# Performance work log

Hardware: AMD Instinct MI355X
Metric: run time of the kernel (lower is better)

## Reference

```python
import jax, jax.numpy as jnp
import numpy as np

EPS = 1e-5
T = 5          # Newton-Schulz iterations
G = 64         # num_groups
FACTOR = 1.0   # reparameterization scale


def setup_inputs() -> dict:
    key = jax.random.key(0)
    k1, k2, k3, k4 = jax.random.split(key, 4)
    B, C, H, W = 32, 256, 64, 64
    x = jax.random.normal(k1, (B, C, H, W), dtype=jnp.float32)
    idx = jax.random.permutation(k2, C)                      # random channel shuffle
    eps1 = jax.random.normal(k3, (B, G, G), dtype=jnp.float32)  # randn_like(wm_inv)
    eps2 = jax.random.normal(k4, (B, G, 1), dtype=jnp.float32)  # randn_like(mean)
    return {"x": x, "idx": idx, "eps1": eps1, "eps2": eps2}


def _sqrtvar(t):
    # torch .var(dim=0) is unbiased (ddof=1); repeat over batch == broadcast
    return jnp.sqrt(jnp.var(t, axis=0, keepdims=True, ddof=1) + EPS)


def reference(x, idx, eps1, eps2):
    B, C, H, W = x.shape
    # reverse permutation: reverse_idx[idx[i]] = i
    reverse_idx = jnp.zeros_like(idx).at[idx].set(jnp.arange(C, dtype=idx.dtype))

    xs = x[:, idx].reshape(B, G, -1)          # [B, G, m], m = (C//G)*H*W
    m = xs.shape[-1]
    mean = xs.mean(-1, keepdims=True)         # [B, G, 1]
    xm = xs - mean

    sigma = jnp.einsum('bgm,bhm->bgh', xm, xm) / m   # [B, G, G]
    I = jnp.eye(G, dtype=x.dtype)
    trace_inv = 1.0 / jnp.trace(sigma, axis1=1, axis2=2)[:, None, None]
    sigma_N = sigma * trace_inv

    # Newton-Schulz inverse square root: P <- 1.5 P - 0.5 P^3 sigma_N
    P = jnp.broadcast_to(I, sigma.shape)
    for _ in range(T):
        P = 1.5 * P - 0.5 * ((P @ P @ P) @ sigma_N)
    wm = P * jnp.sqrt(trace_inv)

    # faithful to original b_inv: solve(I, wm) == wm (original code quirk)
    wm_inv = jnp.linalg.solve(jnp.broadcast_to(I, wm.shape), wm)

    # stochastic reparameterization of gamma (symmetrized via triu) and beta
    wir = wm_inv + (eps1 * FACTOR) * _sqrtvar(wm_inv)
    gamma = jnp.triu(wir) + jnp.swapaxes(jnp.triu(wir, k=1), 1, 2)
    beta = mean + (eps2 * FACTOR) * _sqrtvar(mean)

    y = gamma @ (wm @ xm) + beta              # [B, G, m]
    out = y.reshape(B, C, H, W)[:, reverse_idx]
    return out
```

## Files before the change

### kernel.cpp

```cpp
#include <hip/hip_runtime.h>

typedef __attribute__((ext_vector_type(8))) short short8;
typedef __attribute__((ext_vector_type(4))) short short4v;
typedef __attribute__((ext_vector_type(4))) float f32x4;

#define MFMA16 __builtin_amdgcn_mfma_f32_16x16x32_bf16

__device__ __forceinline__ short bf16t(float f) {
  return (short)(__float_as_uint(f) >> 16);
}
__device__ __forceinline__ float bf16f(short h) {
  return __uint_as_float(((unsigned)(unsigned short)h) << 16);
}

__device__ __forceinline__ void mm64(const float* X, const float* Y, float* D,
                                     int tid) {
  const int R = (tid >> 4) << 2;
  const int Cc = (tid & 15) << 2;
  float acc[4][4];
#pragma unroll
  for (int i = 0; i < 4; i++)
#pragma unroll
    for (int j = 0; j < 4; j++) acc[i][j] = 0.f;
#pragma unroll 4
  for (int kk = 0; kk < 64; kk++) {
    f32x4 a = *(const f32x4*)&X[(kk << 6) + R];
    f32x4 bb = *(const f32x4*)&Y[(kk << 6) + Cc];
#pragma unroll
    for (int i = 0; i < 4; i++)
#pragma unroll
      for (int j = 0; j < 4; j++) acc[i][j] = fmaf(a[i], bb[j], acc[i][j]);
  }
#pragma unroll
  for (int i = 0; i < 4; i++) {
    f32x4 r = {acc[i][0], acc[i][1], acc[i][2], acc[i][3]};
    *(f32x4*)&D[((R + i) << 6) + Cc] = r;
  }
  __syncthreads();
}

__global__ __launch_bounds__(256, 4) void k_stats(const float* __restrict__ x,
                                                  const int* __restrict__ idx,
                                                  float* __restrict__ sigw,
                                                  float* __restrict__ rsum) {
  __shared__ __align__(16) short XT[2][2 * 64 * 72];
  __shared__ int chan[64];
  const int tid = threadIdx.x;
  const int w = tid >> 6, lane = tid & 63;
  const int q = lane >> 4, n15 = lane & 15;
  const int u = tid >> 4;
  const int quad = tid & 15;
  const int blk = blockIdx.x;
  const int b = blk >> 5, k = (blk >> 3) & 3, pc = blk & 7;

  if (tid < 64) chan[tid] = idx[(tid << 2) + k];
  __syncthreads();

  const float* xb = x + ((size_t)b << 20);
  const int pcbase = pc << 9;

  f32x4 acc[4];
#pragma unroll
  for (int t = 0; t < 4; t++) acc[t] = (f32x4){0.f, 0.f, 0.f, 0.f};
  float rsp[4] = {0.f, 0.f, 0.f, 0.f};

  f32x4 vv[4];
#pragma unroll
  for (int i = 0; i < 4; i++)
    vv[i] = *(const f32x4*)&xb[((size_t)chan[(i << 4) + u] << 12) + pcbase +
                               (quad << 2)];

  for (int c = 0; c < 8; c++) {
    short* XH = &XT[c & 1][0];
    short* XL = XH + 64 * 72;
#pragma unroll
    for (int i = 0; i < 4; i++) {
      const int ch = (i << 4) + u;
      rsp[i] += vv[i][0] + vv[i][1] + vv[i][2] + vv[i][3];
      short4v hv, lv;
#pragma unroll
      for (int j = 0; j < 4; j++) {
        hv[j] = bf16t(vv[i][j]);
        lv[j] = bf16t(vv[i][j] - bf16f(hv[j]));
      }
      *(short4v*)&XH[ch * 72 + (quad << 2)] = hv;
      *(short4v*)&XL[ch * 72 + (quad << 2)] = lv;
    }
    if (c < 7) {
      const int p0 = pcbase + ((c + 1) << 6);
#pragma unroll
      for (int i = 0; i < 4; i++)
        vv[i] = *(const f32x4*)&xb[((size_t)chan[(i << 4) + u] << 12) + p0 +
                                   (quad << 2)];
    }
    __syncthreads();
#pragma unroll
    for (int s = 0; s < 2; s++) {
      const int ko = (s << 5) + (q << 3);
      const short8 ah = *(const short8*)&XH[((w << 4) + n15) * 72 + ko];
      const short8 al = *(const short8*)&XL[((w << 4) + n15) * 72 + ko];
#pragma unroll
      for (int hb = 0; hb < 4; hb++) {
        const short8 bh = *(const short8*)&XH[((hb << 4) + n15) * 72 + ko];
        const short8 bl = *(const short8*)&XL[((hb << 4) + n15) * 72 + ko];
        acc[hb] = MFMA16(ah, bh, acc[hb], 0, 0, 0);
        acc[hb] = MFMA16(ah, bl, acc[hb], 0, 0, 0);
        acc[hb] = MFMA16(al, bh, acc[hb], 0, 0, 0);
      }
    }
  }
#pragma unroll
  for (int i = 0; i < 4; i++) {
    float r = rsp[i];
    r += __shfl_xor(r, 1);
    r += __shfl_xor(r, 2);
    r += __shfl_xor(r, 4);
    r += __shfl_xor(r, 8);
    if (quad == 0) atomicAdd(&rsum[(b << 6) + (i << 4) + u], r);
  }
  float* sb = sigw + ((size_t)b << 12);
#pragma unroll
  for (int hb = 0; hb < 4; hb++)
#pragma unroll
    for (int r = 0; r < 4; r++)
      atomicAdd(&sb[(((w << 4) + (q << 2) + r) << 6) + (hb << 4) + n15],
                acc[hb][r]);
}

__global__ __launch_bounds__(256) void k_ns(const float* __restrict__ sigw,
                                            const float* __restrict__ rsum,
                                            float* __restrict__ meanw,
                                            float* __restrict__ wmw) {
  __shared__ __align__(16) float SN[4096];
  __shared__ __align__(16) float Pm[4096];
  __shared__ __align__(16) float Ta[4096];
  __shared__ __align__(16) float Tb[4096];
  __shared__ float ml[64];
  __shared__ float tr_s;
  const int tid = threadIdx.x;
  const int b = blockIdx.x;

  if (tid < 64) {
    const float mu = rsum[(b << 6) + tid] * (1.f / 16384.f);
    ml[tid] = mu;
    meanw[(b << 6) + tid] = mu;
  }
  __syncthreads();
#pragma unroll
  for (int i = 0; i < 16; i++) {
    const int e = (i << 8) + tid;
    const int g = e >> 6, h = e & 63;
    SN[e] = sigw[(b << 12) + e] * (1.f / 16384.f) - ml[g] * ml[h];
  }
  __syncthreads();
  if (tid < 64) {
    float d = SN[tid * 65];
#pragma unroll
    for (int off = 32; off; off >>= 1) d += __shfl_down(d, off);
    if (tid == 0) tr_s = 1.f / d;
  }
  __syncthreads();
  const float trinv = tr_s;
#pragma unroll
  for (int i = 0; i < 16; i++) {
    const int e = (i << 8) + tid;
    SN[e] *= trinv;
    Pm[e] = ((e >> 6) == (e & 63)) ? 1.f : 0.f;
  }
  __syncthreads();

  const int R4 = (tid >> 4) << 2, C4 = (tid & 15) << 2;
  for (int it = 0; it < 5; it++) {
    float p2[4][4], ps[4][4];
#pragma unroll
    for (int i = 0; i < 4; i++)
#pragma unroll
      for (int j = 0; j < 4; j++) {
        p2[i][j] = 0.f;
        ps[i][j] = 0.f;
      }
#pragma unroll 4
    for (int kk = 0; kk < 64; kk++) {
      f32x4 a = *(const f32x4*)&Pm[(kk << 6) + R4];
      f32x4 bp = *(const f32x4*)&Pm[(kk << 6) + C4];
      f32x4 bs = *(const f32x4*)&SN[(kk << 6) + C4];
#pragma unroll
      for (int i = 0; i < 4; i++)
#pragma unroll
        for (int j = 0; j < 4; j++) {
          p2[i][j] = fmaf(a[i], bp[j], p2[i][j]);
          ps[i][j] = fmaf(a[i], bs[j], ps[i][j]);
        }
    }
#pragma unroll
    for (int i = 0; i < 4; i++) {
      f32x4 r1 = {p2[i][0], p2[i][1], p2[i][2], p2[i][3]};
      f32x4 r2 = {ps[i][0], ps[i][1], ps[i][2], ps[i][3]};
      *(f32x4*)&Ta[((R4 + i) << 6) + C4] = r1;
      *(f32x4*)&Tb[((R4 + i) << 6) + C4] = r2;
    }
    __syncthreads();
    float t3[4][4];
#pragma unroll
    for (int i = 0; i < 4; i++)
#pragma unroll
      for (int j = 0; j < 4; j++) t3[i][j] = 0.f;
#pragma unroll 4
    for (int kk = 0; kk < 64; kk++) {
      f32x4 a = *(const f32x4*)&Ta[(kk << 6) + R4];
      f32x4 bb = *(const f32x4*)&Tb[(kk << 6) + C4];
#pragma unroll
      for (int i = 0; i < 4; i++)
#pragma unroll
        for (int j = 0; j < 4; j++) t3[i][j] = fmaf(a[i], bb[j], t3[i][j]);
    }
#pragma unroll
    for (int i = 0; i < 4; i++) {
      f32x4 p = *(const f32x4*)&Pm[((R4 + i) << 6) + C4];
#pragma unroll
      for (int j = 0; j < 4; j++) p[j] = 1.5f * p[j] - 0.5f * t3[i][j];
      *(f32x4*)&Pm[((R4 + i) << 6) + C4] = p;
    }
    __syncthreads();
  }
  const float s = sqrtf(trinv);
#pragma unroll
  for (int i = 0; i < 16; i++) {
    const int e = (i << 8) + tid;
    wmw[(b << 12) + e] = Pm[e] * s;
  }
}

__global__ __launch_bounds__(256) void k_gA(
    const float* __restrict__ wmw, const float* __restrict__ meanw,
    const float* __restrict__ eps1, const float* __restrict__ eps2,
    short* __restrict__ Ahl, float* __restrict__ ofsw) {
  __shared__ __align__(16) float Wl[4096];
  __shared__ __align__(16) float Gm[4096];
  __shared__ __align__(16) float Al[4096];
  __shared__ float ml[64];
  __shared__ float svml[64];
  const int tid = threadIdx.x;
  const int b = blockIdx.x;
  float* Sv = Al;

#pragma unroll
  for (int i = 0; i < 16; i++) {
    const int e = (i << 8) + tid;
    float vv[32];
    float s = 0.f;
#pragma unroll
    for (int p = 0; p < 32; p++) {
      vv[p] = wmw[(p << 12) + e];
      s += vv[p];
    }
    const float mu = s * (1.f / 32.f);
    float s2 = 0.f;
#pragma unroll
    for (int p = 0; p < 32; p++) {
      const float d = vv[p] - mu;
      s2 = fmaf(d, d, s2);
    }
    Sv[e] = sqrtf(s2 * (1.f / 31.f) + 1e-5f);
  }
  if (tid < 64) {
    ml[tid] = meanw[(b << 6) + tid];
    float vv[32];
    float s = 0.f;
#pragma unroll
    for (int p = 0; p < 32; p++) {
      vv[p] = meanw[(p << 6) + tid];
      s += vv[p];
    }
    const float mu = s * (1.f / 32.f);
    float s2 = 0.f;
#pragma unroll
    for (int p = 0; p < 32; p++) {
      const float d = vv[p] - mu;
      s2 = fmaf(d, d, s2);
    }
    svml[tid] = sqrtf(s2 * (1.f / 31.f) + 1e-5f);
  }
#pragma unroll
  for (int i = 0; i < 16; i++) {
    const int e = (i << 8) + tid;
    Wl[e] = wmw[(b << 12) + e];
  }
  __syncthreads();
#pragma unroll
  for (int i = 0; i < 16; i++) {
    const int e = (i << 8) + tid;
    const int g = e >> 6, h = e & 63;
    const int eu = (h >= g) ? e : ((h << 6) + g);
    Gm[e] = Wl[eu] + eps1[(b << 12) + eu] * Sv[eu];
  }
  __syncthreads();
  mm64(Gm, Wl, Al, tid);
  short* Ab = Ahl + ((size_t)b << 13);
#pragma unroll
  for (int i = 0; i < 16; i++) {
    const int e = (i << 8) + tid;
    const float a = Al[e];
    const short h2 = bf16t(a);
    Ab[e] = h2;
    Ab[4096 + e] = bf16t(a - bf16f(h2));
  }
  if (tid < 64) {
    float dot = 0.f;
    for (int h = 0; h < 64; h++) dot = fmaf(Al[(tid << 6) + h], ml[h], dot);
    ofsw[(b << 6) + tid] = ml[tid] + eps2[(b << 6) + tid] * svml[tid] - dot;
  }
}

__global__ __launch_bounds__(256, 4) void k_apply(const float* __restrict__ x,
                                                  const int* __restrict__ idx,
                                                  const short* __restrict__ Ahl,
                                                  const float* __restrict__ ofsw,
                                                  float* __restrict__ out) {
  __shared__ __align__(16) short XT[2][2 * 64 * 72];
  __shared__ int chan[64];
  const int tid = threadIdx.x;
  const int w = tid >> 6, lane = tid & 63;
  const int q = lane >> 4, n15 = lane & 15;
  const int blk = blockIdx.x;
  const int b = blk >> 5, k = (blk >> 3) & 3, pc = blk & 7;

  if (tid < 64) chan[tid] = idx[(tid << 2) + k];

  const short* Ab = Ahl + ((size_t)b << 13);
  short8 ah[2], al[2];
#pragma unroll
  for (int s = 0; s < 2; s++) {
    const int o = (((w << 4) + n15) << 6) + (s << 5) + (q << 3);
    ah[s] = *(const short8*)&Ab[o];
    al[s] = *(const short8*)&Ab[4096 + o];
  }
  const float of = ofsw[(b << 6) + (w << 4) + n15];
  __syncthreads();

  const float* xb = x + ((size_t)b << 20);
  float* outb = out + ((size_t)b << 20);
  const int pcbase = pc << 9;

  float v[16];
#pragma unroll
  for (int j = 0; j < 16; j++)
    v[j] = xb[((size_t)chan[(w << 4) + j] << 12) + pcbase + lane];

  for (int c = 0; c < 8; c++) {
    short* XH = &XT[c & 1][0];
    short* XL = XH + 64 * 72;
#pragma unroll
    for (int jj = 0; jj < 4; jj++) {
      short4v hv, lv;
#pragma unroll
      for (int j = 0; j < 4; j++) {
        const float f = v[(jj << 2) + j];
        hv[j] = bf16t(f);
        lv[j] = bf16t(f - bf16f(hv[j]));
      }
      *(short4v*)&XH[lane * 72 + (w << 4) + (jj << 2)] = hv;
      *(short4v*)&XL[lane * 72 + (w << 4) + (jj << 2)] = lv;
    }
    if (c < 7) {
      const int p0n = pcbase + ((c + 1) << 6);
#pragma unroll
      for (int j = 0; j < 16; j++)
        v[j] = xb[((size_t)chan[(w << 4) + j] << 12) + p0n + lane];
    }
    __syncthreads();

    const int p0 = pcbase + (c << 6);
    f32x4 acc[4];
#pragma unroll
    for (int nb = 0; nb < 4; nb++) acc[nb] = (f32x4){of, of, of, of};
#pragma unroll
    for (int s = 0; s < 2; s++) {
#pragma unroll
      for (int nb = 0; nb < 4; nb++) {
        const int ro = ((nb << 4) + n15) * 72 + (s << 5) + (q << 3);
        const short8 xh = *(const short8*)&XH[ro];
        const short8 xl = *(const short8*)&XL[ro];
        acc[nb] = MFMA16(xh, ah[s], acc[nb], 0, 0, 0);
        acc[nb] = MFMA16(xl, ah[s], acc[nb], 0, 0, 0);
        acc[nb] = MFMA16(xh, al[s], acc[nb], 0, 0, 0);
      }
    }
#pragma unroll
    for (int nb = 0; nb < 4; nb++) {
      *(f32x4*)&outb[((size_t)chan[(w << 4) + n15] << 12) + p0 + (nb << 4) +
                     (q << 2)] = acc[nb];
    }
  }
}

extern "C" void kernel_launch(void* const* d_in, const int* in_sizes, int n_in,
                              void* d_out, int out_size, void* d_ws,
                              size_t ws_size, hipStream_t stream) {
  const float* x = (const float*)d_in[0];
  const int* idx = (const int*)d_in[1];
  const float* eps1 = (const float*)d_in[2];
  const float* eps2 = (const float*)d_in[3];
  float* out = (float*)d_out;
  float* ws = (float*)d_ws;

  float* sigw = ws;
  float* rsum = ws + 131072;
  float* meanw = ws + 133120;
  float* wmw = ws + 135168;
  float* ofsw = ws + 270400;
  short* Ahl = (short*)(ws + 272448);

  hipMemsetAsync(ws, 0, (131072 + 2048) * sizeof(float), stream);
  k_stats<<<1024, 256, 0, stream>>>(x, idx, sigw, rsum);
  k_ns<<<32, 256, 0, stream>>>(sigw, rsum, meanw, wmw);
  k_gA<<<32, 256, 0, stream>>>(wmw, meanw, eps1, eps2, Ahl, ofsw);
  k_apply<<<1024, 256, 0, stream>>>(x, idx, Ahl, ofsw, out);
}
```

Baseline: 320.9 us.

## Move Newton-Schulz iterations to split-bf16 MFMA and peel first iteration

The per-batch Newton-Schulz kernel now computes P@P, P@sigma and the cubic product with bf16 hi/lo split MFMA instructions instead of scalar fp32 FMAs, keeping P in registers for the update. The first iteration is computed in closed form (P0 = 1.5I - 0.5 sigma_N), cutting the matrix iterations from five to four. The two main loops also swap __syncthreads for a barrier that waits only on LDS counters, so outstanding global prefetch loads are not drained. The split-bf16 products carry slightly lower precision than fp32, and this kernel is a small share of total time.

Result: faster. 299.5 us (-6.6%).

```diff
diff --git a/kernel.cpp b/kernel.cpp
--- a/kernel.cpp
+++ b/kernel.cpp
@@ -11,6 +11,12 @@
 }
 __device__ __forceinline__ float bf16f(short h) {
   return __uint_as_float(((unsigned)(unsigned short)h) << 16);
+}
+
+__device__ __forceinline__ void lds_barrier() {
+  asm volatile("s_waitcnt lgkmcnt(0)" ::: "memory");
+  __builtin_amdgcn_s_barrier();
+  asm volatile("" ::: "memory");
 }
 
 __device__ __forceinline__ void mm64(const float* X, const float* Y, float* D,
@@ -93,7 +99,7 @@
         vv[i] = *(const f32x4*)&xb[((size_t)chan[(i << 4) + u] << 12) + p0 +
                                    (quad << 2)];
     }
-    __syncthreads();
+    lds_barrier();
 #pragma unroll
     for (int s = 0; s < 2; s++) {
       const int ko = (s << 5) + (q << 3);
@@ -127,18 +133,23 @@
                 acc[hb][r]);
 }
 
+#define NSTR 72
+
 __global__ __launch_bounds__(256) void k_ns(const float* __restrict__ sigw,
                                             const float* __restrict__ rsum,
                                             float* __restrict__ meanw,
                                             float* __restrict__ wmw) {
-  __shared__ __align__(16) float SN[4096];
-  __shared__ __align__(16) float Pm[4096];
-  __shared__ __align__(16) float Ta[4096];
-  __shared__ __align__(16) float Tb[4096];
+  __shared__ __align__(16) short PA[2 * 64 * NSTR];
+  __shared__ __align__(16) short TB[2 * 64 * NSTR];
+  __shared__ __align__(16) short SB[2 * 64 * NSTR];
   __shared__ float ml[64];
   __shared__ float tr_s;
   const int tid = threadIdx.x;
   const int b = blockIdx.x;
+  const int w = tid >> 6, lane = tid & 63;
+  const int q = lane >> 4, n15 = lane & 15;
+
+  float* SNf = (float*)TB;
 
   if (tid < 64) {
     const float mu = rsum[(b << 6) + tid] * (1.f / 16384.f);
@@ -150,84 +161,125 @@
   for (int i = 0; i < 16; i++) {
     const int e = (i << 8) + tid;
     const int g = e >> 6, h = e & 63;
-    SN[e] = sigw[(b << 12) + e] * (1.f / 16384.f) - ml[g] * ml[h];
+    SNf[e] = sigw[(b << 12) + e] * (1.f / 16384.f) - ml[g] * ml[h];
   }
   __syncthreads();
   if (tid < 64) {
-    float d = SN[tid * 65];
+    float d = SNf[tid * 65];
 #pragma unroll
     for (int off = 32; off; off >>= 1) d += __shfl_down(d, off);
     if (tid == 0) tr_s = 1.f / d;
   }
   __syncthreads();
   const float trinv = tr_s;
-#pragma unroll
-  for (int i = 0; i < 16; i++) {
-    const int e = (i << 8) + tid;
-    SN[e] *= trinv;
-    Pm[e] = ((e >> 6) == (e & 63)) ? 1.f : 0.f;
-  }
-  __syncthreads();
-
-  const int R4 = (tid >> 4) << 2, C4 = (tid & 15) << 2;
-  for (int it = 0; it < 5; it++) {
-    float p2[4][4], ps[4][4];
-#pragma unroll
-    for (int i = 0; i < 4; i++)
-#pragma unroll
-      for (int j = 0; j < 4; j++) {
-        p2[i][j] = 0.f;
-        ps[i][j] = 0.f;
-      }
-#pragma unroll 4
-    for (int kk = 0; kk < 64; kk++) {
-      f32x4 a = *(const f32x4*)&Pm[(kk << 6) + R4];
-      f32x4 bp = *(const f32x4*)&Pm[(kk << 6) + C4];
-      f32x4 bs = *(const f32x4*)&SN[(kk << 6) + C4];
-#pragma unroll
-      for (int i = 0; i < 4; i++)
-#pragma unroll
-        for (int j = 0; j < 4; j++) {
-          p2[i][j] = fmaf(a[i], bp[j], p2[i][j]);
-          ps[i][j] = fmaf(a[i], bs[j], ps[i][j]);
+
+#pragma unroll
+  for (int i = 0; i < 16; i++) {
+    const int e = (i << 8) + tid;
+    const int g = e >> 6, h = e & 63;
+    const float sv = SNf[e] * trinv;
+    const short sh = bf16t(sv);
+    SB[g * NSTR + h] = sh;
+    SB[64 * NSTR + g * NSTR + h] = bf16t(sv - bf16f(sh));
+    const float pv = ((g == h) ? 1.5f : 0.f) - 0.5f * sv;
+    const short ph = bf16t(pv);
+    PA[g * NSTR + h] = ph;
+    PA[64 * NSTR + g * NSTR + h] = bf16t(pv - bf16f(ph));
+  }
+  float pr[4][4];
+#pragma unroll
+  for (int ct = 0; ct < 4; ct++)
+#pragma unroll
+    for (int r = 0; r < 4; r++) {
+      const int row = (w << 4) + (q << 2) + r, col = (ct << 4) + n15;
+      pr[ct][r] =
+          ((row == col) ? 1.5f : 0.f) - 0.5f * SNf[(row << 6) + col] * trinv;
+    }
+  __syncthreads();
+
+  for (int it = 0; it < 4; it++) {
+    f32x4 aP2[4], aPS[4];
+#pragma unroll
+    for (int t = 0; t < 4; t++) {
+      aP2[t] = (f32x4){0.f, 0.f, 0.f, 0.f};
+      aPS[t] = (f32x4){0.f, 0.f, 0.f, 0.f};
+    }
+#pragma unroll
+    for (int s = 0; s < 2; s++) {
+      const int ko = (s << 5) + (q << 3);
+      const short8 ah = *(const short8*)&PA[((w << 4) + n15) * NSTR + ko];
+      const short8 al =
+          *(const short8*)&PA[64 * NSTR + ((w << 4) + n15) * NSTR + ko];
+#pragma unroll
+      for (int ct = 0; ct < 4; ct++) {
+        const short8 bh = *(const short8*)&PA[((ct << 4) + n15) * NSTR + ko];
+        const short8 bl =
+            *(const short8*)&PA[64 * NSTR + ((ct << 4) + n15) * NSTR + ko];
+        aP2[ct] = MFMA16(ah, bh, aP2[ct], 0, 0, 0);
+        aP2[ct] = MFMA16(ah, bl, aP2[ct], 0, 0, 0);
+        aP2[ct] = MFMA16(al, bh, aP2[ct], 0, 0, 0);
+        const short8 ch = *(const short8*)&SB[((ct << 4) + n15) * NSTR + ko];
+        const short8 cl =
+            *(const short8*)&SB[64 * NSTR + ((ct << 4) + n15) * NSTR + ko];
+        aPS[ct] = MFMA16(ah, ch, aPS[ct], 0, 0, 0);
+        aPS[ct] = MFMA16(ah, cl, aPS[ct], 0, 0, 0);
+        aPS[ct] = MFMA16(al, ch, aPS[ct], 0, 0, 0);
+      }
+    }
+    __syncthreads();
+#pragma unroll
+    for (int ct = 0; ct < 4; ct++)
+#pragma unroll
+      for (int r = 0; r < 4; r++) {
+        const int row = (w << 4) + (q << 2) + r, col = (ct << 4) + n15;
+        const float v1 = aP2[ct][r];
+        const short h1 = bf16t(v1);
+        PA[row * NSTR + col] = h1;
+        PA[64 * NSTR + row * NSTR + col] = bf16t(v1 - bf16f(h1));
+        const float v2 = aPS[ct][r];
+        const short h2 = bf16t(v2);
+        TB[row * NSTR + col] = h2;
+        TB[64 * NSTR + row * NSTR + col] = bf16t(v2 - bf16f(h2));
+      }
+    __syncthreads();
+    f32x4 aT3[4];
+#pragma unroll
+    for (int t = 0; t < 4; t++) aT3[t] = (f32x4){0.f, 0.f, 0.f, 0.f};
+#pragma unroll
+    for (int s = 0; s < 2; s++) {
+      const int ko = (s << 5) + (q << 3);
+      const short8 ah = *(const short8*)&PA[((w << 4) + n15) * NSTR + ko];
+      const short8 al =
+          *(const short8*)&PA[64 * NSTR + ((w << 4) + n15) * NSTR + ko];
+#pragma unroll
+      for (int ct = 0; ct < 4; ct++) {
+        const short8 bh = *(const short8*)&TB[((ct << 4) + n15) * NSTR + ko];
+        const short8 bl =
+            *(const short8*)&TB[64 * NSTR + ((ct << 4) + n15) * NSTR + ko];
+        aT3[ct] = MFMA16(ah, bh, aT3[ct], 0, 0, 0);
+        aT3[ct] = MFMA16(ah, bl, aT3[ct], 0, 0, 0);
+        aT3[ct] = MFMA16(al, bh, aT3[ct], 0, 0, 0);
+      }
+    }
+    __syncthreads();
+    const bool last = (it == 3);
+    const float sc = sqrtf(trinv);
+#pragma unroll
+    for (int ct = 0; ct < 4; ct++)
+#pragma unroll
+      for (int r = 0; r < 4; r++) {
+        const int row = (w << 4) + (q << 2) + r, col = (ct << 4) + n15;
+        const float pn = 1.5f * pr[ct][r] - 0.5f * aT3[ct][r];
+        pr[ct][r] = pn;
+        if (last) {
+          wmw[(b << 12) + (row << 6) + col] = pn * sc;
+        } else {
+          const short h1 = bf16t(pn);
+          PA[row * NSTR + col] = h1;
+          PA[64 * NSTR + row * NSTR + col] = bf16t(pn - bf16f(h1));
         }
-    }
-#pragma unroll
-    for (int i = 0; i < 4; i++) {
-      f32x4 r1 = {p2[i][0], p2[i][1], p2[i][2], p2[i][3]};
-      f32x4 r2 = {ps[i][0], ps[i][1], ps[i][2], ps[i][3]};
-      *(f32x4*)&Ta[((R4 + i) << 6) + C4] = r1;
-      *(f32x4*)&Tb[((R4 + i) << 6) + C4] = r2;
-    }
-    __syncthreads();
-    float t3[4][4];
-#pragma unroll
-    for (int i = 0; i < 4; i++)
-#pragma unroll
-      for (int j = 0; j < 4; j++) t3[i][j] = 0.f;
-#pragma unroll 4
-    for (int kk = 0; kk < 64; kk++) {
-      f32x4 a = *(const f32x4*)&Ta[(kk << 6) + R4];
-      f32x4 bb = *(const f32x4*)&Tb[(kk << 6) + C4];
-#pragma unroll
-      for (int i = 0; i < 4; i++)
-#pragma unroll
-        for (int j = 0; j < 4; j++) t3[i][j] = fmaf(a[i], bb[j], t3[i][j]);
-    }
-#pragma unroll
-    for (int i = 0; i < 4; i++) {
-      f32x4 p = *(const f32x4*)&Pm[((R4 + i) << 6) + C4];
-#pragma unroll
-      for (int j = 0; j < 4; j++) p[j] = 1.5f * p[j] - 0.5f * t3[i][j];
-      *(f32x4*)&Pm[((R4 + i) << 6) + C4] = p;
-    }
-    __syncthreads();
-  }
-  const float s = sqrtf(trinv);
-#pragma unroll
-  for (int i = 0; i < 16; i++) {
-    const int e = (i << 8) + tid;
-    wmw[(b << 12) + e] = Pm[e] * s;
+      }
+    if (!last) __syncthreads();
   }
 }
 
@@ -368,7 +420,7 @@
       for (int j = 0; j < 16; j++)
         v[j] = xb[((size_t)chan[(w << 4) + j] << 12) + p0n + lane];
     }
-    __syncthreads();
+    lds_barrier();
 
     const int p0 = pcbase + (c << 6);
     f32x4 acc[4];
```
